# Kernel tuning notes

Hardware: AMD Instinct MI355X
Metric: run time of the kernel (lower is better)

The kernel has to match this reference:

```python
import jax, jax.numpy as jnp
import numpy as np

SEQ, B, NP, NG = 100, 200, 512, 4096

def setup_inputs() -> dict:
    key = jax.random.key(0)
    ks = jax.random.split(key, 6)
    velocity = jax.random.normal(ks[0], (SEQ, B, 2), dtype=jnp.float32)
    init_pc = jax.random.uniform(ks[1], (B, NP), dtype=jnp.float32)
    # encoder: nn.Linear(Np, Ng, bias=False) -> weight (Ng, Np), default kaiming-uniform-ish; use uniform(+-1/sqrt(Np))
    lim_enc = 1.0 / np.sqrt(NP)
    W_enc = jax.random.uniform(ks[2], (NG, NP), minval=-lim_enc, maxval=lim_enc, dtype=jnp.float32)
    # RNN weights: weight_ih_l0 (Ng, 2), weight_hh_l0 (Ng, Ng); torch init uniform(+-1/sqrt(Ng))
    lim = 1.0 / np.sqrt(NG)
    W_ih = jax.random.uniform(ks[3], (NG, 2), minval=-lim, maxval=lim, dtype=jnp.float32)
    W_hh = jax.random.uniform(ks[4], (NG, NG), minval=-lim, maxval=lim, dtype=jnp.float32)
    # decoder: xavier_uniform on (Np, Ng)
    lim_dec = np.sqrt(6.0 / (NP + NG))
    W_dec = jax.random.uniform(ks[5], (NP, NG), minval=-lim_dec, maxval=lim_dec, dtype=jnp.float32)
    return {"velocity": velocity, "init_pc": init_pc, "W_enc": W_enc,
            "W_ih": W_ih, "W_hh": W_hh, "W_dec": W_dec}

def reference(velocity, init_pc, W_enc, W_ih, W_hh, W_dec):
    # h0 = encoder(init_pc): (B, Ng)
    h0 = init_pc @ W_enc.T
    # precompute input projections for all steps: (SEQ, B, Ng)
    vx = jnp.einsum('sbi,gi->sbg', velocity, W_ih)
    def step(h, v_t):
        h_new = jax.nn.relu(v_t + h @ W_hh.T)
        return h_new, h_new
    _, g = jax.lax.scan(step, h0, vx)          # g: (SEQ, B, Ng)
    place_logits = jnp.einsum('sbg,pg->sbp', g, W_dec)  # (SEQ, B, Np)
    return place_logits, g
```

## Files before the change

kernel.cpp:

```cpp
#include <hip/hip_runtime.h>
#include <cstdint>
#include <cstddef>

#define kSEQ 100
#define kB   200
#define kNP  512
#define kNG  4096
#define kMP  256
#define KSPLIT 8

typedef _Float16 f16_t;
typedef f16_t f16x8 __attribute__((ext_vector_type(8)));
typedef f16_t f16x4 __attribute__((ext_vector_type(4)));
typedef float f32x4 __attribute__((ext_vector_type(4)));

__global__ __launch_bounds__(256)
void k_half(const float* __restrict__ src, f16_t* __restrict__ dst, int n8) {
    int i = blockIdx.x * 256 + threadIdx.x;
    if (i >= n8) return;
    const float4* s = (const float4*)src + (size_t)i * 2;
    float4 v0 = s[0], v1 = s[1];
    f16x8 h;
    h[0] = (f16_t)v0.x; h[1] = (f16_t)v0.y; h[2] = (f16_t)v0.z; h[3] = (f16_t)v0.w;
    h[4] = (f16_t)v1.x; h[5] = (f16_t)v1.y; h[6] = (f16_t)v1.z; h[7] = (f16_t)v1.w;
    *(f16x8*)(dst + (size_t)i * 8) = h;
}

__global__ __launch_bounds__(512, 4)
void k_gemm_f16(const f16_t* __restrict__ A, int lda,
                const f16_t* __restrict__ B, int ldb,
                f16_t* __restrict__ part, int kPerChunk) {
    __shared__ __align__(16) f16_t sA[128 * 64];
    __shared__ __align__(16) f16_t sB[128 * 64];

    const int bid    = blockIdx.x;
    const int xcd    = bid & 7;
    const int idx    = bid >> 3;
    const int n_tile = xcd * 4 + (idx & 3);
    const int rem    = idx >> 2;
    const int kc     = rem >> 1;
    const int m_tile = rem & 1;

    const int tid  = threadIdx.x;
    const int lane = tid & 63;
    const int wid  = tid >> 6;
    const int wr   = wid >> 2;
    const int wc   = wid & 3;
    const int m0   = m_tile * 128;
    const int n0   = n_tile * 128;
    const int kBase = kc * kPerChunk;

    f32x4 acc[4][2];
#pragma unroll
    for (int i = 0; i < 4; i++)
#pragma unroll
        for (int j = 0; j < 2; j++) acc[i][j] = (f32x4){0.f, 0.f, 0.f, 0.f};

    const int c0   = tid;
    const int c1   = tid + 512;
    const int r0s  = c0 >> 3, cc0 = c0 & 7;
    const int r1s  = c1 >> 3, cc1 = c1 & 7;
    const unsigned int off0 = ((unsigned)r0s * 128u + (unsigned)cc0 * 16u) ^ (((unsigned)r0s & 7u) << 4);
    const unsigned int off1 = ((unsigned)r1s * 128u + (unsigned)cc1 * 16u) ^ (((unsigned)r1s & 7u) << 4);

    for (int kb = 0; kb < kPerChunk; kb += 64) {
        const int k0 = kBase + kb;
        __syncthreads();
        {
            const uint4* gA0 = (const uint4*)(A + (size_t)(m0 + r0s) * (size_t)lda + k0 + cc0 * 8);
            const uint4* gA1 = (const uint4*)(A + (size_t)(m0 + r1s) * (size_t)lda + k0 + cc1 * 8);
            const uint4* gB0 = (const uint4*)(B + (size_t)(n0 + r0s) * (size_t)ldb + k0 + cc0 * 8);
            const uint4* gB1 = (const uint4*)(B + (size_t)(n0 + r1s) * (size_t)ldb + k0 + cc1 * 8);
            *(uint4*)((char*)sA + off0) = gA0[0];
            *(uint4*)((char*)sA + off1) = gA1[0];
            *(uint4*)((char*)sB + off0) = gB0[0];
            *(uint4*)((char*)sB + off1) = gB1[0];
        }
        __syncthreads();
#pragma unroll
        for (int ks2 = 0; ks2 < 2; ks2++) {
            f16x8 a[4], b[2];
            const unsigned int klane = (unsigned)(lane >> 4) * 16u + (unsigned)ks2 * 64u;
#pragma unroll
            for (int fm = 0; fm < 4; fm++) {
                const unsigned int row = (unsigned)(wr * 64 + fm * 16 + (lane & 15));
                const unsigned int off = (row * 128u + klane) ^ ((row & 7u) << 4);
                a[fm] = *(const f16x8*)((const char*)sA + off);
            }
#pragma unroll
            for (int fn = 0; fn < 2; fn++) {
                const unsigned int row = (unsigned)(wc * 32 + fn * 16 + (lane & 15));
                const unsigned int off = (row * 128u + klane) ^ ((row & 7u) << 4);
                b[fn] = *(const f16x8*)((const char*)sB + off);
            }
#pragma unroll
            for (int fm = 0; fm < 4; fm++)
#pragma unroll
                for (int fn = 0; fn < 2; fn++)
                    acc[fm][fn] = __builtin_amdgcn_mfma_f32_16x16x32_f16(a[fm], b[fn], acc[fm][fn], 0, 0, 0);
        }
    }

    f16_t* po = part + (size_t)kc * ((size_t)kB * kNG);
#pragma unroll
    for (int fm = 0; fm < 4; fm++)
#pragma unroll
        for (int fn = 0; fn < 2; fn++) {
            const int row0 = m0 + wr * 64 + fm * 16 + ((lane >> 4) << 2);
            const int col  = n0 + wc * 32 + fn * 16 + (lane & 15);
#pragma unroll
            for (int j = 0; j < 4; j++) {
                const int row = row0 + j;
                if (row < kB)
                    po[(size_t)row * kNG + col] = (f16_t)acc[fm][fn][j];
            }
        }
}

__global__ __launch_bounds__(256)
void k_reduce(const f16_t* __restrict__ part,
              const float* __restrict__ velocity, const float* __restrict__ W_ih,
              float* __restrict__ gout, f16_t* __restrict__ gb,
              f16_t* __restrict__ hout, int t, int mode) {
    const int b = blockIdx.y;
    const int g = blockIdx.x * 1024 + threadIdx.x * 4;

    float v0 = 0.f, v1 = 0.f, v2 = 0.f, v3 = 0.f;
#pragma unroll
    for (int ks = 0; ks < KSPLIT; ks++) {
        f16x4 p = *(const f16x4*)(part + (size_t)ks * ((size_t)kB * kNG) + (size_t)b * kNG + g);
        v0 += (float)p[0]; v1 += (float)p[1]; v2 += (float)p[2]; v3 += (float)p[3];
    }
    if (mode == 1) {
        const float2 vel = *(const float2*)(velocity + ((size_t)t * kB + b) * 2);
        const float4 w01 = *(const float4*)(W_ih + (size_t)g * 2);
        const float4 w23 = *(const float4*)(W_ih + (size_t)g * 2 + 4);
        v0 = fmaxf(0.f, v0 + vel.x * w01.x + vel.y * w01.y);
        v1 = fmaxf(0.f, v1 + vel.x * w01.z + vel.y * w01.w);
        v2 = fmaxf(0.f, v2 + vel.x * w23.x + vel.y * w23.y);
        v3 = fmaxf(0.f, v3 + vel.x * w23.z + vel.y * w23.w);
        float4 o; o.x = v0; o.y = v1; o.z = v2; o.w = v3;
        *(float4*)(gout + ((size_t)t * kB + b) * kNG + g) = o;
    }
    f16x4 h;
    h[0] = (f16_t)v0; h[1] = (f16_t)v1; h[2] = (f16_t)v2; h[3] = (f16_t)v3;
    *(f16x4*)(hout + (size_t)b * kNG + g) = h;
    if (mode == 1 && gb)
        *(f16x4*)(gb + ((size_t)t * kB + b) * kNG + g) = h;
}

__global__ __launch_bounds__(256)
void k_dec(const float* __restrict__ Gf, const f16_t* __restrict__ Gb,
           const f16_t* __restrict__ Wd, float* __restrict__ out) {
    __shared__ __align__(16) f16_t sA[128 * 64];
    __shared__ __align__(16) f16_t sB[128 * 64];

    const int bid  = blockIdx.x;
    const int xcd  = bid & 7;
    const int idx  = bid >> 3;
    const int tile = xcd * 79 + idx;
    if (tile >= 157 * 4) return;
    const int m0 = (tile >> 2) * 128;
    const int n0 = (tile & 3) * 128;

    const int tid  = threadIdx.x;
    const int lane = tid & 63;
    const int wid  = tid >> 6;
    const int wr   = wid >> 1;
    const int wc   = wid & 1;
    const int M    = kSEQ * kB;

    f32x4 acc[4][4];
#pragma unroll
    for (int i = 0; i < 4; i++)
#pragma unroll
        for (int j = 0; j < 4; j++) acc[i][j] = (f32x4){0.f, 0.f, 0.f, 0.f};

    const int sr   = tid >> 1;
    const int half = tid & 1;
    const int sc   = half * 32;
    const unsigned int swzrow = ((unsigned)sr & 7u) << 4;
    const unsigned int sbase  = (unsigned)sr * 128u + (unsigned)half * 64u;
    int arow = m0 + sr; if (arow > M - 1) arow = M - 1;

    for (int k0 = 0; k0 < kNG; k0 += 64) {
        __syncthreads();
        if (Gb) {
            const uint4* gA = (const uint4*)(Gb + (size_t)arow * kNG + k0 + sc);
#pragma unroll
            for (int i = 0; i < 4; i++) {
                unsigned int off = (sbase + (unsigned)i * 16u) ^ swzrow;
                *(uint4*)((char*)sA + off) = gA[i];
            }
        } else {
            const float4* gA = (const float4*)(Gf + (size_t)arow * kNG + k0 + sc);
#pragma unroll
            for (int i = 0; i < 4; i++) {
                float4 a0 = gA[2 * i], a1 = gA[2 * i + 1];
                f16x8 u;
                u[0] = (f16_t)a0.x; u[1] = (f16_t)a0.y; u[2] = (f16_t)a0.z; u[3] = (f16_t)a0.w;
                u[4] = (f16_t)a1.x; u[5] = (f16_t)a1.y; u[6] = (f16_t)a1.z; u[7] = (f16_t)a1.w;
                unsigned int off = (sbase + (unsigned)i * 16u) ^ swzrow;
                *(f16x8*)((char*)sA + off) = u;
            }
        }
        {
            const uint4* gB = (const uint4*)(Wd + (size_t)(n0 + sr) * kNG + k0 + sc);
#pragma unroll
            for (int i = 0; i < 4; i++) {
                unsigned int off = (sbase + (unsigned)i * 16u) ^ swzrow;
                *(uint4*)((char*)sB + off) = gB[i];
            }
        }
        __syncthreads();
#pragma unroll
        for (int ks2 = 0; ks2 < 2; ks2++) {
            f16x8 a[4], b[4];
            const unsigned int klane = (unsigned)(lane >> 4) * 16u + (unsigned)ks2 * 64u;
#pragma unroll
            for (int fm = 0; fm < 4; fm++) {
                const unsigned int row = (unsigned)(wr * 64 + fm * 16 + (lane & 15));
                const unsigned int off = (row * 128u + klane) ^ ((row & 7u) << 4);
                a[fm] = *(const f16x8*)((const char*)sA + off);
            }
#pragma unroll
            for (int fn = 0; fn < 4; fn++) {
                const unsigned int row = (unsigned)(wc * 64 + fn * 16 + (lane & 15));
                const unsigned int off = (row * 128u + klane) ^ ((row & 7u) << 4);
                b[fn] = *(const f16x8*)((const char*)sB + off);
            }
#pragma unroll
            for (int fm = 0; fm < 4; fm++)
#pragma unroll
                for (int fn = 0; fn < 4; fn++)
                    acc[fm][fn] = __builtin_amdgcn_mfma_f32_16x16x32_f16(a[fm], b[fn], acc[fm][fn], 0, 0, 0);
        }
    }

#pragma unroll
    for (int fm = 0; fm < 4; fm++)
#pragma unroll
        for (int fn = 0; fn < 4; fn++) {
            const int row0 = m0 + wr * 64 + fm * 16 + ((lane >> 4) << 2);
            const int col  = n0 + wc * 64 + fn * 16 + (lane & 15);
#pragma unroll
            for (int j = 0; j < 4; j++) {
                const int row = row0 + j;
                if (row < M) out[(size_t)row * kNP + col] = acc[fm][fn][j];
            }
        }
}

extern "C" void kernel_launch(void* const* d_in, const int* in_sizes, int n_in,
                              void* d_out, int out_size, void* d_ws, size_t ws_size,
                              hipStream_t stream) {
    const float* velocity = (const float*)d_in[0];
    const float* init_pc  = (const float*)d_in[1];
    const float* W_enc    = (const float*)d_in[2];
    const float* W_ih     = (const float*)d_in[3];
    const float* W_hh     = (const float*)d_in[4];
    const float* W_dec    = (const float*)d_in[5];

    float* logits = (float*)d_out;
    float* gout   = logits + (size_t)kSEQ * kB * kNP;

    char* ws = (char*)d_ws;
    size_t off = 0;
    auto alloc = [&](size_t bytes) -> void* {
        void* p = ws + off;
        off += (bytes + 255) & ~(size_t)255;
        return p;
    };
    f16_t* whh  = (f16_t*)alloc((size_t)kNG * kNG * 2);
    f16_t* wdec = (f16_t*)alloc((size_t)kNP * kNG * 2);
    f16_t* wenc = (f16_t*)alloc((size_t)kNG * kNP * 2);
    f16_t* ip   = (f16_t*)alloc((size_t)kMP * kNP * 2);
    f16_t* h_buf[2];
    h_buf[0] = (f16_t*)alloc((size_t)kMP * kNG * 2);
    h_buf[1] = (f16_t*)alloc((size_t)kMP * kNG * 2);
    f16_t* partial = (f16_t*)alloc((size_t)KSPLIT * kB * kNG * 2);
    f16_t* gb = nullptr;
    if (ws_size >= off + (size_t)kSEQ * kB * kNG * 2 + 4096)
        gb = (f16_t*)alloc((size_t)kSEQ * kB * kNG * 2);

    hipMemsetAsync(ip + (size_t)kB * kNP, 0, (size_t)(kMP - kB) * kNP * 2, stream);

    int n8;
    n8 = kNG * kNG / 8;
    k_half<<<(n8 + 255) / 256, 256, 0, stream>>>(W_hh, whh, n8);
    n8 = kNP * kNG / 8;
    k_half<<<(n8 + 255) / 256, 256, 0, stream>>>(W_dec, wdec, n8);
    n8 = kNG * kNP / 8;
    k_half<<<(n8 + 255) / 256, 256, 0, stream>>>(W_enc, wenc, n8);
    n8 = kB * kNP / 8;
    k_half<<<(n8 + 255) / 256, 256, 0, stream>>>(init_pc, ip, n8);

    dim3 gR(4, kB);

    k_gemm_f16<<<512, 512, 0, stream>>>(ip, kNP, wenc, kNP, partial, kNP / KSPLIT);
    k_reduce<<<gR, 256, 0, stream>>>(partial, velocity, W_ih, nullptr, nullptr, h_buf[0], 0, 0);

    int p = 0;
    for (int t = 0; t < kSEQ; t++) {
        k_gemm_f16<<<512, 512, 0, stream>>>(h_buf[p], kNG, whh, kNG, partial, kNG / KSPLIT);
        k_reduce<<<gR, 256, 0, stream>>>(partial, velocity, W_ih, gout, gb, h_buf[p ^ 1], t, 1);
        p ^= 1;
    }

    k_dec<<<632, 256, 0, stream>>>(gout, gb, wdec, logits);
}
```

Baseline: 2.150 ms.

## Use direct global-to-LDS loads and read hidden state from fp16 history buffer

The GEMM tile loads now use the global_load_lds builtin, so 16-byte chunks go straight into shared memory without passing through registers, keeping the same XOR swizzle through a permuted source column. When the fp16 history buffer exists, each step's GEMM reads the previous hidden state directly from that history, and the reduce kernel skips the separate h_buf write, dropping one redundant store per step. The history allocation is padded by kMP rows so the 256-row A reads stay in bounds. This relies on the builtin's per-wave contiguous LDS write layout matching the swizzled addressing.

```diff
diff --git a/kernel.cpp b/kernel.cpp
--- a/kernel.cpp
+++ b/kernel.cpp
@@ -13,6 +13,12 @@
 typedef f16_t f16x8 __attribute__((ext_vector_type(8)));
 typedef f16_t f16x4 __attribute__((ext_vector_type(4)));
 typedef float f32x4 __attribute__((ext_vector_type(4)));
+
+__device__ __forceinline__ void gld_lds16(const f16_t* g, f16_t* l) {
+    __builtin_amdgcn_global_load_lds(
+        (const __attribute__((address_space(1))) unsigned int*)g,
+        (__attribute__((address_space(3))) unsigned int*)l, 16, 0, 0);
+}
 
 __global__ __launch_bounds__(256)
 void k_half(const float* __restrict__ src, f16_t* __restrict__ dst, int n8) {
@@ -56,26 +62,22 @@
 #pragma unroll
         for (int j = 0; j < 2; j++) acc[i][j] = (f32x4){0.f, 0.f, 0.f, 0.f};
 
-    const int c0   = tid;
-    const int c1   = tid + 512;
-    const int r0s  = c0 >> 3, cc0 = c0 & 7;
-    const int r1s  = c1 >> 3, cc1 = c1 & 7;
-    const unsigned int off0 = ((unsigned)r0s * 128u + (unsigned)cc0 * 16u) ^ (((unsigned)r0s & 7u) << 4);
-    const unsigned int off1 = ((unsigned)r1s * 128u + (unsigned)cc1 * 16u) ^ (((unsigned)r1s & 7u) << 4);
+    const int s0   = wid * 128 + lane;
+    const int s1   = s0 + 64;
+    const int r0s  = s0 >> 3, c0 = (s0 & 7) ^ (r0s & 7);
+    const int r1s  = s1 >> 3, c1 = (s1 & 7) ^ (r1s & 7);
+    f16_t* dA0 = sA + (size_t)(wid * 128) * 8;
+    f16_t* dA1 = sA + (size_t)(wid * 128 + 64) * 8;
+    f16_t* dB0 = sB + (size_t)(wid * 128) * 8;
+    f16_t* dB1 = sB + (size_t)(wid * 128 + 64) * 8;
 
     for (int kb = 0; kb < kPerChunk; kb += 64) {
         const int k0 = kBase + kb;
         __syncthreads();
-        {
-            const uint4* gA0 = (const uint4*)(A + (size_t)(m0 + r0s) * (size_t)lda + k0 + cc0 * 8);
-            const uint4* gA1 = (const uint4*)(A + (size_t)(m0 + r1s) * (size_t)lda + k0 + cc1 * 8);
-            const uint4* gB0 = (const uint4*)(B + (size_t)(n0 + r0s) * (size_t)ldb + k0 + cc0 * 8);
-            const uint4* gB1 = (const uint4*)(B + (size_t)(n0 + r1s) * (size_t)ldb + k0 + cc1 * 8);
-            *(uint4*)((char*)sA + off0) = gA0[0];
-            *(uint4*)((char*)sA + off1) = gA1[0];
-            *(uint4*)((char*)sB + off0) = gB0[0];
-            *(uint4*)((char*)sB + off1) = gB1[0];
-        }
+        gld_lds16(A + (size_t)(m0 + r0s) * (size_t)lda + k0 + c0 * 8, dA0);
+        gld_lds16(A + (size_t)(m0 + r1s) * (size_t)lda + k0 + c1 * 8, dA1);
+        gld_lds16(B + (size_t)(n0 + r0s) * (size_t)ldb + k0 + c0 * 8, dB0);
+        gld_lds16(B + (size_t)(n0 + r1s) * (size_t)ldb + k0 + c1 * 8, dB1);
         __syncthreads();
 #pragma unroll
         for (int ks2 = 0; ks2 < 2; ks2++) {
@@ -144,7 +146,8 @@
     }
     f16x4 h;
     h[0] = (f16_t)v0; h[1] = (f16_t)v1; h[2] = (f16_t)v2; h[3] = (f16_t)v3;
-    *(f16x4*)(hout + (size_t)b * kNG + g) = h;
+    if (hout)
+        *(f16x4*)(hout + (size_t)b * kNG + g) = h;
     if (mode == 1 && gb)
         *(f16x4*)(gb + ((size_t)t * kB + b) * kNG + g) = h;
 }
@@ -280,8 +283,8 @@
     h_buf[1] = (f16_t*)alloc((size_t)kMP * kNG * 2);
     f16_t* partial = (f16_t*)alloc((size_t)KSPLIT * kB * kNG * 2);
     f16_t* gb = nullptr;
-    if (ws_size >= off + (size_t)kSEQ * kB * kNG * 2 + 4096)
-        gb = (f16_t*)alloc((size_t)kSEQ * kB * kNG * 2);
+    if (ws_size >= off + ((size_t)kSEQ * kB + kMP) * kNG * 2 + 4096)
+        gb = (f16_t*)alloc(((size_t)kSEQ * kB + kMP) * kNG * 2);
 
     hipMemsetAsync(ip + (size_t)kB * kNP, 0, (size_t)(kMP - kB) * kNP * 2, stream);
 
@@ -300,11 +303,20 @@
     k_gemm_f16<<<512, 512, 0, stream>>>(ip, kNP, wenc, kNP, partial, kNP / KSPLIT);
     k_reduce<<<gR, 256, 0, stream>>>(partial, velocity, W_ih, nullptr, nullptr, h_buf[0], 0, 0);
 
-    int p = 0;
-    for (int t = 0; t < kSEQ; t++) {
-        k_gemm_f16<<<512, 512, 0, stream>>>(h_buf[p], kNG, whh, kNG, partial, kNG / KSPLIT);
-        k_reduce<<<gR, 256, 0, stream>>>(partial, velocity, W_ih, gout, gb, h_buf[p ^ 1], t, 1);
-        p ^= 1;
+    if (gb) {
+        const f16_t* Acur = h_buf[0];
+        for (int t = 0; t < kSEQ; t++) {
+            k_gemm_f16<<<512, 512, 0, stream>>>(Acur, kNG, whh, kNG, partial, kNG / KSPLIT);
+            k_reduce<<<gR, 256, 0, stream>>>(partial, velocity, W_ih, gout, gb, nullptr, t, 1);
+            Acur = gb + (size_t)t * kB * kNG;
+        }
+    } else {
+        int p = 0;
+        for (int t = 0; t < kSEQ; t++) {
+            k_gemm_f16<<<512, 512, 0, stream>>>(h_buf[p], kNG, whh, kNG, partial, kNG / KSPLIT);
+            k_reduce<<<gR, 256, 0, stream>>>(partial, velocity, W_ih, gout, nullptr, h_buf[p ^ 1], t, 1);
+            p ^= 1;
+        }
     }
 
     k_dec<<<632, 256, 0, stream>>>(gout, gb, wdec, logits);
```

New measurement: 2.089 ms. 2.8% less time.
